# Performance work log

Hardware: AMD Instinct MI355X
Metric: run time of the kernel (lower is better)

The kernel has to match this reference:

```python
import jax, jax.numpy as jnp
import numpy as np

NUM_GRAPHS = 2048
NODES_PER_GRAPH = 256
N_NODES = NUM_GRAPHS * NODES_PER_GRAPH
N_EDGES = 2 * N_NODES
F_IN = 768
HID = 128
N_CLS = 2


def setup_inputs() -> dict:
    key = jax.random.key(0)
    ks = jax.random.split(key, 12)
    x = jax.random.normal(ks[0], (N_NODES, F_IN), dtype=jnp.float32)
    edge_index = jax.random.randint(ks[1], (2, N_EDGES), 0, N_NODES, dtype=jnp.int32)
    batch = jnp.repeat(jnp.arange(NUM_GRAPHS, dtype=jnp.int32), NODES_PER_GRAPH)
    s = 1.0 / np.sqrt(F_IN)
    sh = 1.0 / np.sqrt(HID)
    s2h = 1.0 / np.sqrt(2 * HID)
    return {
        "x": x,
        "edge_index": edge_index,
        "batch": batch,
        # SAGEConv: lin_l (aggregated neighbors, with bias) + lin_r (root, no bias)
        "W_l": jax.random.uniform(ks[2], (F_IN, HID), jnp.float32, -s, s),
        "b_l": jax.random.uniform(ks[3], (HID,), jnp.float32, -s, s),
        "W_r": jax.random.uniform(ks[4], (F_IN, HID), jnp.float32, -s, s),
        "W0": jax.random.uniform(ks[5], (F_IN, HID), jnp.float32, -s, s),
        "b0": jax.random.uniform(ks[6], (HID,), jnp.float32, -s, s),
        "W1": jax.random.uniform(ks[7], (2 * HID, HID), jnp.float32, -s2h, s2h),
        "b1": jax.random.uniform(ks[8], (HID,), jnp.float32, -s2h, s2h),
        "W2": jax.random.uniform(ks[9], (HID, N_CLS), jnp.float32, -sh, sh),
        "b2": jax.random.uniform(ks[10], (HID,), jnp.float32, -sh, sh)[:N_CLS],
    }


def reference(x, edge_index, batch, W_l, b_l, W_r, W0, b0, W1, b1, W2, b2):
    n = x.shape[0]
    src, dst = edge_index[0], edge_index[1]
    # SAGEConv with mean aggregation: gather -> segment mean -> transform
    msg_sum = jax.ops.segment_sum(x[src], dst, num_segments=n)      # [N, F]
    cnt = jax.ops.segment_sum(jnp.ones((src.shape[0],), x.dtype), dst, num_segments=n)
    agg = msg_sum / jnp.maximum(cnt, 1.0)[:, None]
    h = jax.nn.relu(agg @ W_l + b_l + x @ W_r)                       # [N, H]
    # global max pool per graph
    pooled = jax.ops.segment_max(h, batch, num_segments=NUM_GRAPHS)  # [G, H]
    # root (news) node = first node of each graph (batch is sorted)
    roots = jnp.searchsorted(batch, jnp.arange(NUM_GRAPHS, dtype=batch.dtype))
    news = jax.nn.relu(x[roots] @ W0 + b0)                           # [G, H]
    z = jax.nn.relu(jnp.concatenate([pooled, news], axis=1) @ W1 + b1)
    return jax.nn.log_softmax(z @ W2 + b2, axis=-1)                  # [G, 2]
```

## Files before the change

kernel.cpp:

```cpp
#include <hip/hip_runtime.h>

#define NGRAPH 2048
#define NPG 256
#define NNODE (NGRAPH*NPG)
#define NEDGE (2*NNODE)
#define FIN 768
#define HID 128
#define SLOTS 64
#define BK 32
#define NKT (FIN/BK)

typedef __bf16 bf16x8 __attribute__((ext_vector_type(8)));
typedef float f32x4 __attribute__((ext_vector_type(4)));

__global__ __launch_bounds__(256) void k_prep(
    const float* __restrict__ Wl, const float* __restrict__ Wr,
    __bf16* __restrict__ WbT, int* __restrict__ deg)
{
    int idx = blockIdx.x * 256 + threadIdx.x;
    deg[idx] = 0;
    if (idx < 256 * FIN) {
        int n = idx / FIN;
        int k = idx - n * FIN;
        float v = (n < HID) ? Wl[k * HID + n] : Wr[k * HID + (n - HID)];
        WbT[idx] = (__bf16)v;
    }
}

__global__ __launch_bounds__(512, 1) void k_gemm(
    const float* __restrict__ X, const __bf16* __restrict__ WbT,
    __bf16* __restrict__ Yl, __bf16* __restrict__ Yr,
    const int* __restrict__ ei, int* __restrict__ deg, int* __restrict__ elist)
{
    __shared__ __align__(16) char sm[65536];
    const int t = threadIdx.x;

    {
        int e = blockIdx.x * 512 + t;
        int src = ei[e];
        int dst = ei[NEDGE + e];
        int pos = atomicAdd(deg + dst, 1);
        if (pos < SLOTS) elist[(size_t)pos * NNODE + dst] = src;
    }

    const int lane = t & 63;
    const int w = t >> 6;
    const int wr = w >> 2;
    const int wc = w & 3;
    const size_t node0 = (size_t)blockIdx.x * 256;

    f32x4 acc[8][4];
#pragma unroll
    for (int m = 0; m < 8; ++m)
#pragma unroll
        for (int n = 0; n < 4; ++n)
            acc[m][n] = (f32x4){0.f, 0.f, 0.f, 0.f};

    const int arow = t >> 1;
    const int ak = (t & 1) * 16;
    const float* asrc = X + (node0 + arow) * FIN + ak;
    const int axr = ((arow >> 1) & 3) << 4;
    const int aoff0 = arow * 64 + ((ak * 2) ^ axr);
    const int aoff1 = arow * 64 + ((ak * 2 + 16) ^ axr);

#define STAGE_B(k0, dst)                                                    \
    {                                                                       \
        _Pragma("unroll")                                                   \
        for (int r = 0; r < 2; ++r) {                                       \
            int idx = r * 512 + t;                                          \
            int bn = idx >> 2;                                              \
            int bj = idx & 3;                                               \
            int koff = (bj ^ ((bn >> 1) & 3)) << 3;                         \
            const __bf16* g = WbT + bn * FIN + (k0) + koff;                 \
            __builtin_amdgcn_global_load_lds(                               \
                (__attribute__((address_space(1))) void*)g,                 \
                (__attribute__((address_space(3))) void*)((dst) + idx * 16),\
                16, 0, 0);                                                  \
        }                                                                   \
    }

    {
        const f32x4* s4 = (const f32x4*)asrc;
        f32x4 p0 = s4[0], p1 = s4[1], p2 = s4[2], p3 = s4[3];
        STAGE_B(0, sm + 32768);
        bf16x8 h0, h1;
#pragma unroll
        for (int i = 0; i < 4; ++i) {
            h0[i]     = (__bf16)p0[i];
            h0[4 + i] = (__bf16)p1[i];
            h1[i]     = (__bf16)p2[i];
            h1[4 + i] = (__bf16)p3[i];
        }
        *(bf16x8*)(sm + aoff0) = h0;
        *(bf16x8*)(sm + aoff1) = h1;
    }
    __syncthreads();

    int cur = 0;
    for (int kt = 0; kt < NKT; ++kt) {
        char* sAc = sm + cur * 16384;
        char* sBc = sm + 32768 + cur * 16384;
        char* sAn = sm + (cur ^ 1) * 16384;
        char* sBn = sm + 32768 + (cur ^ 1) * 16384;
        const bool more = (kt + 1 < NKT);

        f32x4 q0, q1, q2, q3;
        if (more) {
            const f32x4* s4 = (const f32x4*)(asrc + (kt + 1) * BK);
            q0 = s4[0]; q1 = s4[1]; q2 = s4[2]; q3 = s4[3];
            STAGE_B((kt + 1) * BK, sBn);
        }

        const int kb = (lane >> 4) << 4;
        bf16x8 a[8], b[4];
#pragma unroll
        for (int m = 0; m < 8; ++m) {
            int row = wr * 128 + m * 16 + (lane & 15);
            a[m] = *(const bf16x8*)(sAc + row * 64 + (kb ^ (((row >> 1) & 3) << 4)));
        }
#pragma unroll
        for (int n = 0; n < 4; ++n) {
            int row = wc * 64 + n * 16 + (lane & 15);
            b[n] = *(const bf16x8*)(sBc + row * 64 + (kb ^ (((row >> 1) & 3) << 4)));
        }
#pragma unroll
        for (int m = 0; m < 8; ++m)
#pragma unroll
            for (int n = 0; n < 4; ++n)
                acc[m][n] = __builtin_amdgcn_mfma_f32_16x16x32_bf16(
                    a[m], b[n], acc[m][n], 0, 0, 0);

        if (more) {
            bf16x8 h0, h1;
#pragma unroll
            for (int i = 0; i < 4; ++i) {
                h0[i]     = (__bf16)q0[i];
                h0[4 + i] = (__bf16)q1[i];
                h1[i]     = (__bf16)q2[i];
                h1[4 + i] = (__bf16)q3[i];
            }
            *(bf16x8*)(sAn + aoff0) = h0;
            *(bf16x8*)(sAn + aoff1) = h1;
        }
        __syncthreads();
        cur ^= 1;
    }

#pragma unroll
    for (int m = 0; m < 8; ++m) {
        const int rbase = wr * 128 + m * 16 + ((lane >> 4) << 2);
#pragma unroll
        for (int n = 0; n < 4; ++n) {
            const int col = wc * 64 + n * 16 + (lane & 15);
            __bf16* dst = (col < HID) ? Yl : Yr;
            const int c = col & (HID - 1);
#pragma unroll
            for (int j = 0; j < 4; ++j)
                dst[(node0 + rbase + j) * HID + c] = (__bf16)acc[m][n][j];
        }
    }
#undef STAGE_B
}

__global__ __launch_bounds__(512) void k_hpool_news(
    const int* __restrict__ deg, const int* __restrict__ elist,
    const __bf16* __restrict__ Yl, const __bf16* __restrict__ Yr,
    const float* __restrict__ bl, const float* __restrict__ X,
    const float* __restrict__ W0, const float* __restrict__ b0,
    float* __restrict__ pooled, float* __restrict__ news)
{
    __shared__ __align__(16) char smraw[12288];
    const int b = blockIdx.x;
    const int t = threadIdx.x;
    if (b < NGRAPH) {
        const int g = b;
        int* sdeg = (int*)smraw;
        int* sel  = (int*)(smraw + 1024);
        float* red = (float*)(smraw + 5120);
        if (t < 256) sdeg[t] = deg[(size_t)g * NPG + t];
#pragma unroll
        for (int r = 0; r < 2; ++r) {
            int idx = r * 512 + t;
            int j = idx >> 8, i = idx & 255;
            sel[idx] = elist[(size_t)j * NNODE + (size_t)g * NPG + i];
        }
        __syncthreads();
        const int l = t & 63;
        const int sub = t >> 6;
        const int d2 = l * 2;
        const float bl0 = bl[d2], bl1 = bl[d2 + 1];
        const unsigned short* yl = (const unsigned short*)Yl;
        const unsigned short* yr = (const unsigned short*)Yr;
        float m0 = -3.0e38f, m1 = -3.0e38f;
        for (int i = sub; i < NPG; i += 8) {
            const size_t node = (size_t)g * NPG + i;
            const int dg = sdeg[i];
            const int dgc = dg < SLOTS ? dg : SLOTS;
            float s0 = 0.f, s1 = 0.f;
            const int d4 = dgc < 4 ? dgc : 4;
            for (int j = 0; j < d4; ++j) {
                int srcn = sel[j * 256 + i];
                unsigned v = *(const unsigned*)(yl + (size_t)srcn * HID + d2);
                s0 += __uint_as_float((v & 0xffffu) << 16);
                s1 += __uint_as_float(v & 0xffff0000u);
            }
            for (int j = 4; j < dgc; ++j) {
                int srcn = elist[(size_t)j * NNODE + node];
                unsigned v = *(const unsigned*)(yl + (size_t)srcn * HID + d2);
                s0 += __uint_as_float((v & 0xffffu) << 16);
                s1 += __uint_as_float(v & 0xffff0000u);
            }
            unsigned vy = *(const unsigned*)(yr + node * HID + d2);
            float inv = 1.f / fmaxf((float)dg, 1.f);
            float h0 = s0 * inv + bl0 + __uint_as_float((vy & 0xffffu) << 16);
            float h1 = s1 * inv + bl1 + __uint_as_float(vy & 0xffff0000u);
            m0 = fmaxf(m0, fmaxf(h0, 0.f));
            m1 = fmaxf(m1, fmaxf(h1, 0.f));
        }
        red[sub * 128 + d2] = m0;
        red[sub * 128 + d2 + 1] = m1;
        __syncthreads();
        if (t < 128) {
            float v = red[t];
#pragma unroll
            for (int s = 1; s < 8; ++s) v = fmaxf(v, red[s * 128 + t]);
            pooled[(size_t)g * HID + t] = v;
        }
    } else {
        const int g = (b - NGRAPH) * 4 + (t >> 7);
        const int d = t & 127;
        float* xs = (float*)smraw + (t >> 7) * FIN;
        const float* xrow = X + (size_t)g * NPG * FIN;
        for (int i = d; i < FIN; i += 128) xs[i] = xrow[i];
        __syncthreads();
        float a0 = 0.f, a1 = 0.f, a2 = 0.f, a3 = 0.f;
        for (int k = 0; k < FIN; k += 4) {
            a0 = fmaf(xs[k + 0], W0[(k + 0) * HID + d], a0);
            a1 = fmaf(xs[k + 1], W0[(k + 1) * HID + d], a1);
            a2 = fmaf(xs[k + 2], W0[(k + 2) * HID + d], a2);
            a3 = fmaf(xs[k + 3], W0[(k + 3) * HID + d], a3);
        }
        news[(size_t)g * HID + d] = fmaxf((a0 + a1) + (a2 + a3) + b0[d], 0.f);
    }
}

__global__ __launch_bounds__(128) void k_mlp(
    const float* __restrict__ pooled, const float* __restrict__ news,
    const float* __restrict__ W1, const float* __restrict__ b1,
    const float* __restrict__ W2, const float* __restrict__ b2,
    float* __restrict__ out)
{
    __shared__ float cat[2 * HID];
    __shared__ float zs[HID];
    const int g = blockIdx.x, d = threadIdx.x;
    cat[d] = pooled[(size_t)g * HID + d];
    cat[HID + d] = news[(size_t)g * HID + d];
    __syncthreads();
    float a0 = 0.f, a1 = 0.f, a2 = 0.f, a3 = 0.f;
    for (int k = 0; k < 2 * HID; k += 4) {
        a0 = fmaf(cat[k + 0], W1[(k + 0) * HID + d], a0);
        a1 = fmaf(cat[k + 1], W1[(k + 1) * HID + d], a1);
        a2 = fmaf(cat[k + 2], W1[(k + 2) * HID + d], a2);
        a3 = fmaf(cat[k + 3], W1[(k + 3) * HID + d], a3);
    }
    zs[d] = fmaxf((a0 + a1) + (a2 + a3) + b1[d], 0.f);
    __syncthreads();
    if (d == 0) {
        float l0 = b2[0], l1 = b2[1];
        for (int k = 0; k < HID; ++k) {
            float z = zs[k];
            l0 = fmaf(z, W2[k * 2 + 0], l0);
            l1 = fmaf(z, W2[k * 2 + 1], l1);
        }
        float mx = fmaxf(l0, l1);
        float lse = mx + logf(expf(l0 - mx) + expf(l1 - mx));
        out[(size_t)g * 2 + 0] = l0 - lse;
        out[(size_t)g * 2 + 1] = l1 - lse;
    }
}

extern "C" void kernel_launch(void* const* d_in, const int* in_sizes, int n_in,
                              void* d_out, int out_size, void* d_ws, size_t ws_size,
                              hipStream_t stream)
{
    const float* x   = (const float*)d_in[0];
    const int*   ei  = (const int*)d_in[1];
    const float* W_l = (const float*)d_in[3];
    const float* b_l = (const float*)d_in[4];
    const float* W_r = (const float*)d_in[5];
    const float* W0  = (const float*)d_in[6];
    const float* b0  = (const float*)d_in[7];
    const float* W1  = (const float*)d_in[8];
    const float* b1  = (const float*)d_in[9];
    const float* W2  = (const float*)d_in[10];
    const float* b2  = (const float*)d_in[11];
    float* out = (float*)d_out;

    char* ws = (char*)d_ws;
    size_t off = 0;
    auto alloc = [&](size_t bytes) {
        char* p = ws + off;
        off += (bytes + 511) & ~(size_t)511;
        return p;
    };
    __bf16* WbT   = (__bf16*)alloc((size_t)256 * FIN * 2);
    __bf16* Yl    = (__bf16*)alloc((size_t)NNODE * HID * 2);
    __bf16* Yr    = (__bf16*)alloc((size_t)NNODE * HID * 2);
    int*    deg   = (int*)alloc((size_t)NNODE * 4);
    int*    elist = (int*)alloc((size_t)NNODE * SLOTS * 4);
    float*  pooled= (float*)alloc((size_t)NGRAPH * HID * 4);
    float*  news  = (float*)alloc((size_t)NGRAPH * HID * 4);
    if (off > ws_size) return;

    k_prep<<<NNODE / 256, 256, 0, stream>>>(W_l, W_r, WbT, deg);
    k_gemm<<<NNODE / 256, 512, 0, stream>>>(x, WbT, Yl, Yr, ei, deg, elist);
    k_hpool_news<<<NGRAPH + NGRAPH / 4, 512, 0, stream>>>(
        deg, elist, Yl, Yr, b_l, x, W0, b0, pooled, news);
    k_mlp<<<NGRAPH, 128, 0, stream>>>(pooled, news, W1, b1, W2, b2, out);
}
```

Baseline: 702.1 us.

## Fuse pooling, news projection and MLP head into one per-graph kernel

Merges the pooling/news kernel and the MLP kernel into a single per-graph block. The news GEMV is split across four thread groups along K, and the W2 dot product uses a wavefront shuffle reduction. The gather loop now handles two nodes per iteration with branchless masked loads for the first four neighbours to raise memory-level parallelism. This removes one launch and the pooled/news round trip through global memory, at the cost of more shared memory and idle threads during the MLP tail.

```diff
diff --git a/kernel.cpp b/kernel.cpp
--- a/kernel.cpp
+++ b/kernel.cpp
@@ -12,6 +12,13 @@
 
 typedef __bf16 bf16x8 __attribute__((ext_vector_type(8)));
 typedef float f32x4 __attribute__((ext_vector_type(4)));
+
+__device__ __forceinline__ float bflo(unsigned v) {
+    return __uint_as_float((v & 0xffffu) << 16);
+}
+__device__ __forceinline__ float bfhi(unsigned v) {
+    return __uint_as_float(v & 0xffff0000u);
+}
 
 __global__ __launch_bounds__(256) void k_prep(
     const float* __restrict__ Wl, const float* __restrict__ Wr,
@@ -162,120 +169,153 @@
 #undef STAGE_B
 }
 
-__global__ __launch_bounds__(512) void k_hpool_news(
+__global__ __launch_bounds__(512) void k_fused(
     const int* __restrict__ deg, const int* __restrict__ elist,
     const __bf16* __restrict__ Yl, const __bf16* __restrict__ Yr,
     const float* __restrict__ bl, const float* __restrict__ X,
     const float* __restrict__ W0, const float* __restrict__ b0,
-    float* __restrict__ pooled, float* __restrict__ news)
+    const float* __restrict__ W1, const float* __restrict__ b1,
+    const float* __restrict__ W2, const float* __restrict__ b2,
+    float* __restrict__ out)
 {
-    __shared__ __align__(16) char smraw[12288];
-    const int b = blockIdx.x;
+    __shared__ int   sdeg[NPG];
+    __shared__ int   sel[4 * NPG];
+    __shared__ float xs[FIN];
+    __shared__ float red[8 * HID];
+    __shared__ float nred[4 * HID];
+    __shared__ float cat[2 * HID];
+    __shared__ float zs[HID];
+
+    const int g = blockIdx.x;
     const int t = threadIdx.x;
-    if (b < NGRAPH) {
-        const int g = b;
-        int* sdeg = (int*)smraw;
-        int* sel  = (int*)(smraw + 1024);
-        float* red = (float*)(smraw + 5120);
-        if (t < 256) sdeg[t] = deg[(size_t)g * NPG + t];
-#pragma unroll
-        for (int r = 0; r < 2; ++r) {
-            int idx = r * 512 + t;
-            int j = idx >> 8, i = idx & 255;
-            sel[idx] = elist[(size_t)j * NNODE + (size_t)g * NPG + i];
-        }
-        __syncthreads();
-        const int l = t & 63;
-        const int sub = t >> 6;
-        const int d2 = l * 2;
-        const float bl0 = bl[d2], bl1 = bl[d2 + 1];
-        const unsigned short* yl = (const unsigned short*)Yl;
-        const unsigned short* yr = (const unsigned short*)Yr;
-        float m0 = -3.0e38f, m1 = -3.0e38f;
-        for (int i = sub; i < NPG; i += 8) {
-            const size_t node = (size_t)g * NPG + i;
-            const int dg = sdeg[i];
-            const int dgc = dg < SLOTS ? dg : SLOTS;
-            float s0 = 0.f, s1 = 0.f;
-            const int d4 = dgc < 4 ? dgc : 4;
-            for (int j = 0; j < d4; ++j) {
-                int srcn = sel[j * 256 + i];
-                unsigned v = *(const unsigned*)(yl + (size_t)srcn * HID + d2);
-                s0 += __uint_as_float((v & 0xffffu) << 16);
-                s1 += __uint_as_float(v & 0xffff0000u);
+    const size_t gbase = (size_t)g * NPG;
+
+    if (t < NPG) sdeg[t] = deg[gbase + t];
+#pragma unroll
+    for (int r = 0; r < 2; ++r) {
+        int idx = r * 512 + t;
+        sel[idx] = elist[(size_t)(idx >> 8) * NNODE + gbase + (idx & 255)];
+    }
+    for (int i = t; i < FIN; i += 512) xs[i] = X[gbase * FIN + i];
+    __syncthreads();
+
+    const int l = t & 63;
+    const int sub = t >> 6;
+    const int d2 = l * 2;
+    const float bl0 = bl[d2], bl1 = bl[d2 + 1];
+    const unsigned short* yl = (const unsigned short*)Yl;
+    const unsigned short* yr = (const unsigned short*)Yr;
+    float m0 = -3.0e38f, m1 = -3.0e38f;
+
+    for (int i0 = sub; i0 < NPG; i0 += 16) {
+        const int iA = i0, iB = i0 + 8;
+        const int dgA = sdeg[iA], dgB = sdeg[iB];
+        unsigned vA[4], vB[4];
+        float mkA[4], mkB[4];
+#pragma unroll
+        for (int j = 0; j < 4; ++j) {
+            int sA = sel[j * NPG + iA];
+            int sB = sel[j * NPG + iB];
+            mkA[j] = (j < dgA) ? 1.f : 0.f;
+            mkB[j] = (j < dgB) ? 1.f : 0.f;
+            sA = (j < dgA) ? sA : 0;
+            sB = (j < dgB) ? sB : 0;
+            vA[j] = *(const unsigned*)(yl + (size_t)sA * HID + d2);
+            vB[j] = *(const unsigned*)(yl + (size_t)sB * HID + d2);
+        }
+        const unsigned vyA = *(const unsigned*)(yr + (gbase + iA) * HID + d2);
+        const unsigned vyB = *(const unsigned*)(yr + (gbase + iB) * HID + d2);
+        float s0A = 0.f, s1A = 0.f, s0B = 0.f, s1B = 0.f;
+#pragma unroll
+        for (int j = 0; j < 4; ++j) {
+            s0A = fmaf(mkA[j], bflo(vA[j]), s0A);
+            s1A = fmaf(mkA[j], bfhi(vA[j]), s1A);
+            s0B = fmaf(mkB[j], bflo(vB[j]), s0B);
+            s1B = fmaf(mkB[j], bfhi(vB[j]), s1B);
+        }
+        if (dgA > 4) {
+            const int dgc = dgA < SLOTS ? dgA : SLOTS;
+            for (int j = 4; j < dgc; ++j) {
+                int s = elist[(size_t)j * NNODE + gbase + iA];
+                unsigned v = *(const unsigned*)(yl + (size_t)s * HID + d2);
+                s0A += bflo(v); s1A += bfhi(v);
             }
+        }
+        if (dgB > 4) {
+            const int dgc = dgB < SLOTS ? dgB : SLOTS;
             for (int j = 4; j < dgc; ++j) {
-                int srcn = elist[(size_t)j * NNODE + node];
-                unsigned v = *(const unsigned*)(yl + (size_t)srcn * HID + d2);
-                s0 += __uint_as_float((v & 0xffffu) << 16);
-                s1 += __uint_as_float(v & 0xffff0000u);
+                int s = elist[(size_t)j * NNODE + gbase + iB];
+                unsigned v = *(const unsigned*)(yl + (size_t)s * HID + d2);
+                s0B += bflo(v); s1B += bfhi(v);
             }
-            unsigned vy = *(const unsigned*)(yr + node * HID + d2);
-            float inv = 1.f / fmaxf((float)dg, 1.f);
-            float h0 = s0 * inv + bl0 + __uint_as_float((vy & 0xffffu) << 16);
-            float h1 = s1 * inv + bl1 + __uint_as_float(vy & 0xffff0000u);
-            m0 = fmaxf(m0, fmaxf(h0, 0.f));
-            m1 = fmaxf(m1, fmaxf(h1, 0.f));
-        }
-        red[sub * 128 + d2] = m0;
-        red[sub * 128 + d2 + 1] = m1;
-        __syncthreads();
-        if (t < 128) {
-            float v = red[t];
-#pragma unroll
-            for (int s = 1; s < 8; ++s) v = fmaxf(v, red[s * 128 + t]);
-            pooled[(size_t)g * HID + t] = v;
-        }
-    } else {
-        const int g = (b - NGRAPH) * 4 + (t >> 7);
+        }
+        const float invA = 1.f / fmaxf((float)dgA, 1.f);
+        const float invB = 1.f / fmaxf((float)dgB, 1.f);
+        float h0 = fmaf(s0A, invA, bl0) + bflo(vyA);
+        float h1 = fmaf(s1A, invA, bl1) + bfhi(vyA);
+        m0 = fmaxf(m0, fmaxf(h0, 0.f));
+        m1 = fmaxf(m1, fmaxf(h1, 0.f));
+        h0 = fmaf(s0B, invB, bl0) + bflo(vyB);
+        h1 = fmaf(s1B, invB, bl1) + bfhi(vyB);
+        m0 = fmaxf(m0, fmaxf(h0, 0.f));
+        m1 = fmaxf(m1, fmaxf(h1, 0.f));
+    }
+    red[sub * HID + d2] = m0;
+    red[sub * HID + d2 + 1] = m1;
+
+    {
+        const int q = t >> 7;
         const int d = t & 127;
-        float* xs = (float*)smraw + (t >> 7) * FIN;
-        const float* xrow = X + (size_t)g * NPG * FIN;
-        for (int i = d; i < FIN; i += 128) xs[i] = xrow[i];
-        __syncthreads();
+        const int kb = q * 192;
         float a0 = 0.f, a1 = 0.f, a2 = 0.f, a3 = 0.f;
-        for (int k = 0; k < FIN; k += 4) {
+        for (int k = kb; k < kb + 192; k += 4) {
             a0 = fmaf(xs[k + 0], W0[(k + 0) * HID + d], a0);
             a1 = fmaf(xs[k + 1], W0[(k + 1) * HID + d], a1);
             a2 = fmaf(xs[k + 2], W0[(k + 2) * HID + d], a2);
             a3 = fmaf(xs[k + 3], W0[(k + 3) * HID + d], a3);
         }
-        news[(size_t)g * HID + d] = fmaxf((a0 + a1) + (a2 + a3) + b0[d], 0.f);
-    }
-}
-
-__global__ __launch_bounds__(128) void k_mlp(
-    const float* __restrict__ pooled, const float* __restrict__ news,
-    const float* __restrict__ W1, const float* __restrict__ b1,
-    const float* __restrict__ W2, const float* __restrict__ b2,
-    float* __restrict__ out)
-{
-    __shared__ float cat[2 * HID];
-    __shared__ float zs[HID];
-    const int g = blockIdx.x, d = threadIdx.x;
-    cat[d] = pooled[(size_t)g * HID + d];
-    cat[HID + d] = news[(size_t)g * HID + d];
-    __syncthreads();
-    float a0 = 0.f, a1 = 0.f, a2 = 0.f, a3 = 0.f;
-    for (int k = 0; k < 2 * HID; k += 4) {
-        a0 = fmaf(cat[k + 0], W1[(k + 0) * HID + d], a0);
-        a1 = fmaf(cat[k + 1], W1[(k + 1) * HID + d], a1);
-        a2 = fmaf(cat[k + 2], W1[(k + 2) * HID + d], a2);
-        a3 = fmaf(cat[k + 3], W1[(k + 3) * HID + d], a3);
-    }
-    zs[d] = fmaxf((a0 + a1) + (a2 + a3) + b1[d], 0.f);
-    __syncthreads();
-    if (d == 0) {
-        float l0 = b2[0], l1 = b2[1];
-        for (int k = 0; k < HID; ++k) {
-            float z = zs[k];
-            l0 = fmaf(z, W2[k * 2 + 0], l0);
-            l1 = fmaf(z, W2[k * 2 + 1], l1);
-        }
-        float mx = fmaxf(l0, l1);
-        float lse = mx + logf(expf(l0 - mx) + expf(l1 - mx));
-        out[(size_t)g * 2 + 0] = l0 - lse;
-        out[(size_t)g * 2 + 1] = l1 - lse;
+        nred[q * HID + d] = (a0 + a1) + (a2 + a3);
+    }
+    __syncthreads();
+
+    if (t < HID) {
+        float v = red[t];
+#pragma unroll
+        for (int s = 1; s < 8; ++s) v = fmaxf(v, red[s * HID + t]);
+        cat[t] = v;
+        float nw = (nred[t] + nred[HID + t]) + (nred[2 * HID + t] + nred[3 * HID + t]);
+        cat[HID + t] = fmaxf(nw + b0[t], 0.f);
+    }
+    __syncthreads();
+
+    if (t < HID) {
+        float a0 = 0.f, a1 = 0.f, a2 = 0.f, a3 = 0.f;
+        for (int k = 0; k < 2 * HID; k += 4) {
+            a0 = fmaf(cat[k + 0], W1[(k + 0) * HID + t], a0);
+            a1 = fmaf(cat[k + 1], W1[(k + 1) * HID + t], a1);
+            a2 = fmaf(cat[k + 2], W1[(k + 2) * HID + t], a2);
+            a3 = fmaf(cat[k + 3], W1[(k + 3) * HID + t], a3);
+        }
+        zs[t] = fmaxf((a0 + a1) + (a2 + a3) + b1[t], 0.f);
+    }
+    __syncthreads();
+
+    if (t < 64) {
+        float z0 = zs[t * 2], z1 = zs[t * 2 + 1];
+        float p0 = fmaf(z0, W2[t * 4 + 0], z1 * W2[t * 4 + 2]);
+        float p1 = fmaf(z0, W2[t * 4 + 1], z1 * W2[t * 4 + 3]);
+#pragma unroll
+        for (int off = 32; off; off >>= 1) {
+            p0 += __shfl_down(p0, off);
+            p1 += __shfl_down(p1, off);
+        }
+        if (t == 0) {
+            float l0 = p0 + b2[0], l1 = p1 + b2[1];
+            float mx = fmaxf(l0, l1);
+            float lse = mx + logf(expf(l0 - mx) + expf(l1 - mx));
+            out[(size_t)g * 2 + 0] = l0 - lse;
+            out[(size_t)g * 2 + 1] = l1 - lse;
+        }
     }
 }
 
@@ -308,13 +348,10 @@
     __bf16* Yr    = (__bf16*)alloc((size_t)NNODE * HID * 2);
     int*    deg   = (int*)alloc((size_t)NNODE * 4);
     int*    elist = (int*)alloc((size_t)NNODE * SLOTS * 4);
-    float*  pooled= (float*)alloc((size_t)NGRAPH * HID * 4);
-    float*  news  = (float*)alloc((size_t)NGRAPH * HID * 4);
     if (off > ws_size) return;
 
     k_prep<<<NNODE / 256, 256, 0, stream>>>(W_l, W_r, WbT, deg);
     k_gemm<<<NNODE / 256, 512, 0, stream>>>(x, WbT, Yl, Yr, ei, deg, elist);
-    k_hpool_news<<<NGRAPH + NGRAPH / 4, 512, 0, stream>>>(
-        deg, elist, Yl, Yr, b_l, x, W0, b0, pooled, news);
-    k_mlp<<<NGRAPH, 128, 0, stream>>>(pooled, news, W1, b1, W2, b2, out);
-}
+    k_fused<<<NGRAPH, 512, 0, stream>>>(deg, elist, Yl, Yr, b_l, x, W0, b0,
+                                        W1, b1, W2, b2, out);
+}
```

Result: faster. 635.8 us (-9.4%).
